# Optimization experiments

Hardware: AMD Instinct MI355X
Metric: run time of the kernel (lower is better)

## Reference

```python
import jax, jax.numpy as jnp
import numpy as np

K = 16  # neighbors
EPS = 1e-3  # Keras BatchNormalization default epsilon


def _bn(x, gamma, beta, mean, var):
    return (x - mean) * jax.lax.rsqrt(var + EPS) * gamma + beta


def setup_inputs() -> dict:
    key = jax.random.key(0)
    ks = jax.random.split(key, 16)
    B, P, C = 128, 256, 64
    inp = {
        "points": jax.random.normal(ks[0], (B, P, 3), jnp.float32),
        "features": jax.random.normal(ks[1], (B, P, C), jnp.float32),
        "w0": jax.random.normal(ks[2], (2 * C, 64), jnp.float32) * 0.08,
        "w1": jax.random.normal(ks[3], (64, 64), jnp.float32) * 0.12,
        "w2": jax.random.normal(ks[4], (64, 64), jnp.float32) * 0.12,
        "gammas": 0.8 + 0.4 * jax.random.uniform(ks[5], (3, 64), jnp.float32),
        "betas": 0.1 * jax.random.normal(ks[6], (3, 64), jnp.float32),
        "means": 0.1 * jax.random.normal(ks[7], (3, 64), jnp.float32),
        "variances": 0.5 + jax.random.uniform(ks[8], (3, 64), jnp.float32),
        "sc_w": jax.random.normal(ks[9], (C, 64), jnp.float32) * 0.12,
        "sc_gamma": 0.8 + 0.4 * jax.random.uniform(ks[10], (64,), jnp.float32),
        "sc_beta": 0.1 * jax.random.normal(ks[11], (64,), jnp.float32),
        "sc_mean": 0.1 * jax.random.normal(ks[12], (64,), jnp.float32),
        "sc_var": 0.5 + jax.random.uniform(ks[13], (64,), jnp.float32),
    }
    return inp


def reference(points, features, w0, w1, w2, gammas, betas, means, variances,
              sc_w, sc_gamma, sc_beta, sc_mean, sc_var):
    B, P, C = features.shape
    # pairwise squared-distance matrix: ||a||^2 - 2 a.b + ||b||^2  -> [B, P, P]
    r = jnp.sum(points * points, axis=2, keepdims=True)  # [B, P, 1]
    m = jnp.einsum('bpc,bqc->bpq', points, points)
    d = r - 2.0 * m + jnp.swapaxes(r, 1, 2)
    # top_k of -d: K+1 nearest (incl. self at position 0), drop self
    _, idx = jax.lax.top_k(-d, K + 1)
    idx = idx[:, :, 1:]  # [B, P, K]
    # KNN gather of features
    knn_fts = features[jnp.arange(B)[:, None, None], idx]  # [B, P, K, C]
    center = jnp.broadcast_to(features[:, :, None, :], (B, P, K, C))
    x = jnp.concatenate([center, knn_fts - center], axis=-1)  # [B, P, K, 2C]
    # per-edge MLP: 1x1 conv + BN (inference) + relu
    for i, w in enumerate((w0, w1, w2)):
        x = jnp.einsum('bpkc,cd->bpkd', x, w)
        x = _bn(x, gammas[i], betas[i], means[i], variances[i])
        x = jax.nn.relu(x)
    fts = jnp.mean(x, axis=2)  # average pooling over neighbors -> [B, P, 64]
    # shortcut 1x1 conv + BN
    sc = jnp.einsum('bpc,cd->bpd', features, sc_w)
    sc = _bn(sc, sc_gamma, sc_beta, sc_mean, sc_var)
    return jax.nn.relu(sc + fts)
```

## Files before the change

kernel.cpp:

```cpp
#include <hip/hip_runtime.h>
#include <math.h>

#define NBATCH 128
#define NP 256
#define NC 64
#define KNN 16
#define EPSV 1e-3f

typedef __bf16 bf16_t;
typedef bf16_t bf16x8 __attribute__((ext_vector_type(8)));
typedef float f32x4 __attribute__((ext_vector_type(4)));
typedef unsigned short u16x4 __attribute__((ext_vector_type(4)));

static __device__ __forceinline__ f32x4 mfma16(bf16x8 a, bf16x8 b, f32x4 c) {
    return __builtin_amdgcn_mfma_f32_16x16x32_bf16(a, b, c, 0, 0, 0);
}
static __device__ __forceinline__ unsigned short f2bfu(float f) {
    union { bf16_t b; unsigned short u; } cv; cv.b = (bf16_t)f; return cv.u;
}
static __device__ __forceinline__ unsigned umin2(unsigned a, unsigned b) { return a < b ? a : b; }
static __device__ __forceinline__ unsigned umax2(unsigned a, unsigned b) { return a > b ? a : b; }

#define CFENCE() asm volatile("" ::: "memory")

#define INSERTK(k_)                                                   \
    do {                                                              \
        _Pragma("unroll")                                             \
        for (int ii = KNN - 1; ii >= 1; --ii)                         \
            bk[ii] = umin2(umax2((k_), bk[ii - 1]), bk[ii]);          \
        bk[0] = umin2((k_), bk[0]);                                   \
    } while (0)

__global__ __launch_bounds__(256) void knn_kernel(const float* __restrict__ points,
                                                  int* __restrict__ idx_out) {
    const int bb = blockIdx.x >> 1;
    const int qbase = (blockIdx.x & 1) * 128;
    const int t = threadIdx.x;
    const int qt = t & 127;
    const int half = t >> 7;
    const int p = qbase + qt;

    __shared__ __align__(16) float4 sp[NP];
    __shared__ unsigned sk[128][17];

    const float* pb = points + (size_t)bb * NP * 3;
    sp[t] = make_float4(pb[t * 3 + 0], pb[t * 3 + 1], pb[t * 3 + 2], 0.f);
    __syncthreads();

    const float4 qp = sp[p];
    unsigned bk[KNN];
#pragma unroll
    for (int i = 0; i < KNN; ++i) bk[i] = 0xFFFFFFFFu;

    const int cbase = half * 128;
#pragma unroll 4
    for (int c = 0; c < 128; ++c) {
        const int cand = cbase + c;
        const float4 P = sp[cand];
        const float dx = qp.x - P.x, dy = qp.y - P.y, dz = qp.z - P.z;
        const float d = fmaf(dx, dx, fmaf(dy, dy, dz * dz));
        unsigned key = (__float_as_uint(d) & 0xFFFFFF00u) | (unsigned)cand;
        key = (cand == p) ? 0xFFFFFFFFu : key;
        INSERTK(key);
    }

    if (half == 1) {
#pragma unroll
        for (int i = 0; i < KNN; ++i) sk[qt][i] = bk[i];
    }
    __syncthreads();
    if (half == 0) {
        for (int j = 0; j < KNN; ++j) {
            const unsigned key = sk[qt][j];
            if (key >= bk[KNN - 1]) break;
            INSERTK(key);
        }
        int* op = idx_out + ((size_t)bb * NP + p) * KNN;
#pragma unroll
        for (int i = 0; i < KNN; ++i) op[i] = (int)(bk[i] & 0xFFu);
    }
}

__global__ __launch_bounds__(256) void fcvt_kernel(const float* __restrict__ f,
                                                   unsigned short* __restrict__ o) {
    const int tid = blockIdx.x * 256 + threadIdx.x;
    const float4 a = ((const float4*)f)[tid * 2];
    const float4 b = ((const float4*)f)[tid * 2 + 1];
    union { unsigned short s[8]; uint4 v; } r;
    r.s[0] = f2bfu(a.x); r.s[1] = f2bfu(a.y); r.s[2] = f2bfu(a.z); r.s[3] = f2bfu(a.w);
    r.s[4] = f2bfu(b.x); r.s[5] = f2bfu(b.y); r.s[6] = f2bfu(b.z); r.s[7] = f2bfu(b.w);
    ((uint4*)o)[tid] = r.v;
}

__global__ __launch_bounds__(256) void prep_kernel(
    const float* __restrict__ w0, const float* __restrict__ w1,
    const float* __restrict__ w2, const float* __restrict__ sc_w,
    const float* __restrict__ gammas, const float* __restrict__ betas,
    const float* __restrict__ means, const float* __restrict__ variances,
    const float* __restrict__ sc_gamma, const float* __restrict__ sc_beta,
    const float* __restrict__ sc_mean, const float* __restrict__ sc_var,
    unsigned short* __restrict__ wsf, float* __restrict__ bnp)
{
    const int tid = blockIdx.x * 256 + threadIdx.x;
    if (tid < 20480) {
        const int region = tid >> 12;
        const int e2 = tid & 4095;
        const int f = e2 >> 9;
        const int r = e2 & 511;
        const int lane = r >> 3, j = r & 7;
        const int ks = f >> 2, t = f & 3;
        const int row = ks * 32 + (lane >> 4) * 8 + j;
        const int col = 4 * (lane & 15) + t;
        float v;
        if (region == 0)      v = w0[row * 64 + col] - w0[(64 + row) * 64 + col];
        else if (region == 1) v = w0[(64 + row) * 64 + col];
        else if (region == 2) v = w1[row * 64 + col];
        else if (region == 3) v = w2[row * 64 + col];
        else                  v = sc_w[row * 64 + col];
        wsf[tid] = f2bfu(v);
    } else {
        const int e = tid - 20480;
        if (e < 192) {
            float s = gammas[e] * rsqrtf(variances[e] + EPSV);
            bnp[e] = s;
            bnp[192 + e] = betas[e] - means[e] * s;
        } else if (e < 256) {
            const int d = e - 192;
            float s = sc_gamma[d] * rsqrtf(sc_var[d] + EPSV);
            bnp[384 + d] = s;
            bnp[448 + d] = sc_beta[d] - sc_mean[d] * s;
        }
    }
}

__global__ __launch_bounds__(256) void edge_kernel(
    const unsigned short* __restrict__ fbf, const int* __restrict__ knn_idx,
    const unsigned short* __restrict__ wsf, const float* __restrict__ bnp,
    float* __restrict__ out)
{
    __shared__ __align__(16) unsigned short slab[4][16 * 72];
    __shared__ __align__(16) float s0buf[4][8][64];
    __shared__ __align__(16) float ftsbuf[4][8][64];

    const int tid = threadIdx.x;
    const int wid = tid >> 6;
    const int l = tid & 63;
    const int i = l & 15;
    const int h = l >> 4;
    const int wg = (blockIdx.x & 7) * 128 + (blockIdx.x >> 3);
    const int p0 = (wg * 4 + wid) * 8;
    const int b = p0 >> 8;

    unsigned short* sl = slab[wid];

    const bf16x8* __restrict__ WV = (const bf16x8*)(wsf);
    const bf16x8* __restrict__ W0H = (const bf16x8*)(wsf + 4096);
    const bf16x8* __restrict__ W1 = (const bf16x8*)(wsf + 8192);
    const bf16x8* __restrict__ W2 = (const bf16x8*)(wsf + 12288);

    bf16x8 w0h[2][4], w1r[2][4], w2r[2][4];
#pragma unroll
    for (int ks = 0; ks < 2; ++ks)
#pragma unroll
        for (int t = 0; t < 4; ++t) {
            w0h[ks][t] = W0H[(ks * 4 + t) * 64 + l];
            w1r[ks][t] = W1[(ks * 4 + t) * 64 + l];
            w2r[ks][t] = W2[(ks * 4 + t) * 64 + l];
        }

    float4 scl[3], shf[3];
#pragma unroll
    for (int L = 0; L < 3; ++L) {
        scl[L] = *(const float4*)&bnp[L * 64 + 4 * i];
        shf[L] = *(const float4*)&bnp[192 + L * 64 + 4 * i];
    }

    {
        const unsigned short* cp = fbf + (size_t)(p0 + (i & 7)) * NC;
        bf16x8 a0 = *(const bf16x8*)(cp + 8 * h);
        bf16x8 a1 = *(const bf16x8*)(cp + 32 + 8 * h);
        f32x4 acc[4];
#pragma unroll
        for (int t = 0; t < 4; ++t) {
            f32x4 z = {0.f, 0.f, 0.f, 0.f};
            z = mfma16(a0, WV[t * 64 + l], z);
            acc[t] = mfma16(a1, WV[(4 + t) * 64 + l], z);
        }
        if (h < 2) {
#pragma unroll
            for (int r = 0; r < 4; ++r) {
                float4 v = make_float4(acc[0][r], acc[1][r], acc[2][r], acc[3][r]);
                *(float4*)&s0buf[wid][h * 4 + r][4 * i] = v;
            }
        }
    }
    int nks[8];
#pragma unroll
    for (int q = 0; q < 8; ++q) nks[q] = knn_idx[(size_t)(p0 + q) * KNN + i];
    CFENCE();

    bf16x8 fc0, fc1;
    {
        const unsigned short* sp = fbf + (size_t)(b * NP + nks[0]) * NC;
        fc0 = *(const bf16x8*)(sp + 8 * h);
        fc1 = *(const bf16x8*)(sp + 32 + 8 * h);
    }

#pragma unroll
    for (int q = 0; q < 8; ++q) {
        float4 s0q = *(const float4*)&s0buf[wid][q][4 * i];
        {
            f32x4 acc[4];
#pragma unroll
            for (int t = 0; t < 4; ++t) {
                f32x4 z = {0.f, 0.f, 0.f, 0.f};
                z = mfma16(fc0, w0h[0][t], z);
                acc[t] = mfma16(fc1, w0h[1][t], z);
            }
            const float* sp_ = (const float*)&s0q;
            const float* sc_ = (const float*)&scl[0];
            const float* sh_ = (const float*)&shf[0];
#pragma unroll
            for (int r = 0; r < 4; ++r) {
                u16x4 pk;
#pragma unroll
                for (int t = 0; t < 4; ++t)
                    pk[t] = f2bfu(fmaxf(fmaf(acc[t][r] + sp_[t], sc_[t], sh_[t]), 0.f));
                *(u16x4*)&sl[(h * 4 + r) * 72 + 4 * i] = pk;
            }
        }
        bf16x8 fn0, fn1;
        if (q < 7) {
            const unsigned short* sp = fbf + (size_t)(b * NP + nks[(q + 1) & 7]) * NC;
            fn0 = *(const bf16x8*)(sp + 8 * h);
            fn1 = *(const bf16x8*)(sp + 32 + 8 * h);
        }
        CFENCE();

        {
            bf16x8 x0 = *(const bf16x8*)(sl + i * 72 + h * 8);
            bf16x8 x1 = *(const bf16x8*)(sl + i * 72 + h * 8 + 32);
            f32x4 acc[4];
#pragma unroll
            for (int t = 0; t < 4; ++t) {
                f32x4 z = {0.f, 0.f, 0.f, 0.f};
                z = mfma16(x0, w1r[0][t], z);
                acc[t] = mfma16(x1, w1r[1][t], z);
            }
            const float* sc_ = (const float*)&scl[1];
            const float* sh_ = (const float*)&shf[1];
#pragma unroll
            for (int r = 0; r < 4; ++r) {
                u16x4 pk;
#pragma unroll
                for (int t = 0; t < 4; ++t)
                    pk[t] = f2bfu(fmaxf(fmaf(acc[t][r], sc_[t], sh_[t]), 0.f));
                *(u16x4*)&sl[(h * 4 + r) * 72 + 4 * i] = pk;
            }
        }
        CFENCE();

        {
            bf16x8 x0 = *(const bf16x8*)(sl + i * 72 + h * 8);
            bf16x8 x1 = *(const bf16x8*)(sl + i * 72 + h * 8 + 32);
            const float* sc_ = (const float*)&scl[2];
            const float* sh_ = (const float*)&shf[2];
            float st[4];
#pragma unroll
            for (int t = 0; t < 4; ++t) {
                f32x4 z = {0.f, 0.f, 0.f, 0.f};
                z = mfma16(x0, w2r[0][t], z);
                f32x4 acc = mfma16(x1, w2r[1][t], z);
                float s = 0.f;
#pragma unroll
                for (int r = 0; r < 4; ++r)
                    s += fmaxf(fmaf(acc[r], sc_[t], sh_[t]), 0.f);
                s += __shfl_xor(s, 16, 64);
                s += __shfl_xor(s, 32, 64);
                st[t] = s * (1.f / 16.f);
            }
            if (h == 0)
                *(float4*)&ftsbuf[wid][q][4 * i] =
                    make_float4(st[0], st[1], st[2], st[3]);
        }
        CFENCE();
        fc0 = fn0; fc1 = fn1;
    }

    {
        const bf16x8* __restrict__ WS = (const bf16x8*)(wsf + 16384);
        float4 sscl = *(const float4*)&bnp[384 + 4 * i];
        float4 sshf = *(const float4*)&bnp[448 + 4 * i];
        const unsigned short* fp = fbf + (size_t)(p0 + (i & 7)) * NC;
        bf16x8 a0 = *(const bf16x8*)(fp + 8 * h);
        bf16x8 a1 = *(const bf16x8*)(fp + 32 + 8 * h);
        f32x4 acc[4];
#pragma unroll
        for (int t = 0; t < 4; ++t) {
            f32x4 z = {0.f, 0.f, 0.f, 0.f};
            z = mfma16(a0, WS[t * 64 + l], z);
            acc[t] = mfma16(a1, WS[(4 + t) * 64 + l], z);
        }
        if (h < 2) {
            const float* ss_ = (const float*)&sscl;
            const float* sf_ = (const float*)&sshf;
#pragma unroll
            for (int r = 0; r < 4; ++r) {
                const int q = h * 4 + r;
                float4 fts = *(const float4*)&ftsbuf[wid][q][4 * i];
                const float* ft_ = (const float*)&fts;
                float4 o;
                float* o_ = (float*)&o;
#pragma unroll
                for (int t = 0; t < 4; ++t)
                    o_[t] = fmaxf(fmaf(acc[t][r], ss_[t], sf_[t]) + ft_[t], 0.f);
                *(float4*)&out[(size_t)(p0 + q) * NC + 4 * i] = o;
            }
        }
    }
}

extern "C" void kernel_launch(void* const* d_in, const int* in_sizes, int n_in,
                              void* d_out, int out_size, void* d_ws, size_t ws_size,
                              hipStream_t stream) {
    const float* points    = (const float*)d_in[0];
    const float* features  = (const float*)d_in[1];
    const float* w0        = (const float*)d_in[2];
    const float* w1        = (const float*)d_in[3];
    const float* w2        = (const float*)d_in[4];
    const float* gammas    = (const float*)d_in[5];
    const float* betas     = (const float*)d_in[6];
    const float* means     = (const float*)d_in[7];
    const float* variances = (const float*)d_in[8];
    const float* sc_w      = (const float*)d_in[9];
    const float* sc_gamma  = (const float*)d_in[10];
    const float* sc_beta   = (const float*)d_in[11];
    const float* sc_mean   = (const float*)d_in[12];
    const float* sc_var    = (const float*)d_in[13];
    float* out = (float*)d_out;

    int* knn_buf = (int*)d_ws;
    unsigned short* fbf = (unsigned short*)((char*)d_ws + (1 << 21));
    unsigned short* wsf = (unsigned short*)((char*)d_ws + (3 << 21));
    float* bnp = (float*)((char*)d_ws + (3 << 21) + 40960);

    prep_kernel<<<81, 256, 0, stream>>>(w0, w1, w2, sc_w, gammas, betas, means,
                                        variances, sc_gamma, sc_beta, sc_mean,
                                        sc_var, wsf, bnp);
    fcvt_kernel<<<1024, 256, 0, stream>>>(features, fbf);
    knn_kernel<<<NBATCH * 2, 256, 0, stream>>>(points, knn_buf);
    edge_kernel<<<NBATCH * NP / 32, 256, 0, stream>>>(fbf, knn_buf, wsf, bnp, out);
}
```

Baseline: 52.70 us.

## Merge setup kernels into one launch and process point pairs in edge kernel

Three preparatory kernels (weight/BN prep, feature bf16 conversion, KNN search) are combined into one launch whose work is split by block index, cutting launch overhead and letting the independent pieces run concurrently. The edge kernel now handles two points per iteration, loading both neighbor sets up front and interleaving their MFMA chains through a double LDS slab, which exposes more instruction-level parallelism. The single-point software prefetch of the next point's neighbors is dropped, and the pair processing raises register and LDS use, which could lower occupancy.

```diff
diff --git a/kernel.cpp b/kernel.cpp
--- a/kernel.cpp
+++ b/kernel.cpp
@@ -31,104 +31,103 @@
         bk[0] = umin2((k_), bk[0]);                                   \
     } while (0)
 
-__global__ __launch_bounds__(256) void knn_kernel(const float* __restrict__ points,
-                                                  int* __restrict__ idx_out) {
-    const int bb = blockIdx.x >> 1;
-    const int qbase = (blockIdx.x & 1) * 128;
-    const int t = threadIdx.x;
-    const int qt = t & 127;
-    const int half = t >> 7;
-    const int p = qbase + qt;
-
-    __shared__ __align__(16) float4 sp[NP];
-    __shared__ unsigned sk[128][17];
-
-    const float* pb = points + (size_t)bb * NP * 3;
-    sp[t] = make_float4(pb[t * 3 + 0], pb[t * 3 + 1], pb[t * 3 + 2], 0.f);
-    __syncthreads();
-
-    const float4 qp = sp[p];
-    unsigned bk[KNN];
-#pragma unroll
-    for (int i = 0; i < KNN; ++i) bk[i] = 0xFFFFFFFFu;
-
-    const int cbase = half * 128;
-#pragma unroll 4
-    for (int c = 0; c < 128; ++c) {
-        const int cand = cbase + c;
-        const float4 P = sp[cand];
-        const float dx = qp.x - P.x, dy = qp.y - P.y, dz = qp.z - P.z;
-        const float d = fmaf(dx, dx, fmaf(dy, dy, dz * dz));
-        unsigned key = (__float_as_uint(d) & 0xFFFFFF00u) | (unsigned)cand;
-        key = (cand == p) ? 0xFFFFFFFFu : key;
-        INSERTK(key);
-    }
-
-    if (half == 1) {
-#pragma unroll
-        for (int i = 0; i < KNN; ++i) sk[qt][i] = bk[i];
-    }
-    __syncthreads();
-    if (half == 0) {
-        for (int j = 0; j < KNN; ++j) {
-            const unsigned key = sk[qt][j];
-            if (key >= bk[KNN - 1]) break;
-            INSERTK(key);
-        }
-        int* op = idx_out + ((size_t)bb * NP + p) * KNN;
-#pragma unroll
-        for (int i = 0; i < KNN; ++i) op[i] = (int)(bk[i] & 0xFFu);
-    }
-}
-
-__global__ __launch_bounds__(256) void fcvt_kernel(const float* __restrict__ f,
-                                                   unsigned short* __restrict__ o) {
-    const int tid = blockIdx.x * 256 + threadIdx.x;
-    const float4 a = ((const float4*)f)[tid * 2];
-    const float4 b = ((const float4*)f)[tid * 2 + 1];
-    union { unsigned short s[8]; uint4 v; } r;
-    r.s[0] = f2bfu(a.x); r.s[1] = f2bfu(a.y); r.s[2] = f2bfu(a.z); r.s[3] = f2bfu(a.w);
-    r.s[4] = f2bfu(b.x); r.s[5] = f2bfu(b.y); r.s[6] = f2bfu(b.z); r.s[7] = f2bfu(b.w);
-    ((uint4*)o)[tid] = r.v;
-}
-
-__global__ __launch_bounds__(256) void prep_kernel(
+__global__ __launch_bounds__(256) void setup_kernel(
+    const float* __restrict__ points, const float* __restrict__ features,
     const float* __restrict__ w0, const float* __restrict__ w1,
     const float* __restrict__ w2, const float* __restrict__ sc_w,
     const float* __restrict__ gammas, const float* __restrict__ betas,
     const float* __restrict__ means, const float* __restrict__ variances,
     const float* __restrict__ sc_gamma, const float* __restrict__ sc_beta,
     const float* __restrict__ sc_mean, const float* __restrict__ sc_var,
-    unsigned short* __restrict__ wsf, float* __restrict__ bnp)
+    unsigned short* __restrict__ fbf, unsigned short* __restrict__ wsf,
+    float* __restrict__ bnp, int* __restrict__ knn_out)
 {
-    const int tid = blockIdx.x * 256 + threadIdx.x;
-    if (tid < 20480) {
-        const int region = tid >> 12;
-        const int e2 = tid & 4095;
-        const int f = e2 >> 9;
-        const int r = e2 & 511;
-        const int lane = r >> 3, j = r & 7;
-        const int ks = f >> 2, t = f & 3;
-        const int row = ks * 32 + (lane >> 4) * 8 + j;
-        const int col = 4 * (lane & 15) + t;
-        float v;
-        if (region == 0)      v = w0[row * 64 + col] - w0[(64 + row) * 64 + col];
-        else if (region == 1) v = w0[(64 + row) * 64 + col];
-        else if (region == 2) v = w1[row * 64 + col];
-        else if (region == 3) v = w2[row * 64 + col];
-        else                  v = sc_w[row * 64 + col];
-        wsf[tid] = f2bfu(v);
+    const int bid = blockIdx.x;
+    if (bid < 1024) {
+        const int tid = bid * 256 + threadIdx.x;
+        const float4 a = ((const float4*)features)[tid * 2];
+        const float4 b = ((const float4*)features)[tid * 2 + 1];
+        union { unsigned short s[8]; uint4 v; } r;
+        r.s[0] = f2bfu(a.x); r.s[1] = f2bfu(a.y); r.s[2] = f2bfu(a.z); r.s[3] = f2bfu(a.w);
+        r.s[4] = f2bfu(b.x); r.s[5] = f2bfu(b.y); r.s[6] = f2bfu(b.z); r.s[7] = f2bfu(b.w);
+        ((uint4*)fbf)[tid] = r.v;
+    } else if (bid < 1105) {
+        const int tid = (bid - 1024) * 256 + threadIdx.x;
+        if (tid < 20480) {
+            const int region = tid >> 12;
+            const int e2 = tid & 4095;
+            const int f = e2 >> 9;
+            const int r = e2 & 511;
+            const int lane = r >> 3, j = r & 7;
+            const int ks = f >> 2, t = f & 3;
+            const int row = ks * 32 + (lane >> 4) * 8 + j;
+            const int col = 4 * (lane & 15) + t;
+            float v;
+            if (region == 0)      v = w0[row * 64 + col] - w0[(64 + row) * 64 + col];
+            else if (region == 1) v = w0[(64 + row) * 64 + col];
+            else if (region == 2) v = w1[row * 64 + col];
+            else if (region == 3) v = w2[row * 64 + col];
+            else                  v = sc_w[row * 64 + col];
+            wsf[tid] = f2bfu(v);
+        } else {
+            const int e = tid - 20480;
+            if (e < 192) {
+                float s = gammas[e] * rsqrtf(variances[e] + EPSV);
+                bnp[e] = s;
+                bnp[192 + e] = betas[e] - means[e] * s;
+            } else if (e < 256) {
+                const int d = e - 192;
+                float s = sc_gamma[d] * rsqrtf(sc_var[d] + EPSV);
+                bnp[384 + d] = s;
+                bnp[448 + d] = sc_beta[d] - sc_mean[d] * s;
+            }
+        }
     } else {
-        const int e = tid - 20480;
-        if (e < 192) {
-            float s = gammas[e] * rsqrtf(variances[e] + EPSV);
-            bnp[e] = s;
-            bnp[192 + e] = betas[e] - means[e] * s;
-        } else if (e < 256) {
-            const int d = e - 192;
-            float s = sc_gamma[d] * rsqrtf(sc_var[d] + EPSV);
-            bnp[384 + d] = s;
-            bnp[448 + d] = sc_beta[d] - sc_mean[d] * s;
+        __shared__ __align__(16) float4 sp[NP];
+        __shared__ unsigned sk[128][17];
+        const int kb = bid - 1105;
+        const int bb = kb >> 1;
+        const int qbase = (kb & 1) * 128;
+        const int t = threadIdx.x;
+        const int qt = t & 127;
+        const int half = t >> 7;
+        const int p = qbase + qt;
+
+        const float* pb = points + (size_t)bb * NP * 3;
+        sp[t] = make_float4(pb[t * 3 + 0], pb[t * 3 + 1], pb[t * 3 + 2], 0.f);
+        __syncthreads();
+
+        const float4 qp = sp[p];
+        unsigned bk[KNN];
+#pragma unroll
+        for (int i = 0; i < KNN; ++i) bk[i] = 0xFFFFFFFFu;
+
+        const int cbase = half * 128;
+#pragma unroll 4
+        for (int c = 0; c < 128; ++c) {
+            const int cand = cbase + c;
+            const float4 P = sp[cand];
+            const float dx = qp.x - P.x, dy = qp.y - P.y, dz = qp.z - P.z;
+            const float d = fmaf(dx, dx, fmaf(dy, dy, dz * dz));
+            unsigned key = (__float_as_uint(d) & 0xFFFFFF00u) | (unsigned)cand;
+            key = (cand == p) ? 0xFFFFFFFFu : key;
+            INSERTK(key);
+        }
+
+        if (half == 1) {
+#pragma unroll
+            for (int i = 0; i < KNN; ++i) sk[qt][i] = bk[i];
+        }
+        __syncthreads();
+        if (half == 0) {
+            for (int j = 0; j < KNN; ++j) {
+                const unsigned key = sk[qt][j];
+                if (key >= bk[KNN - 1]) break;
+                INSERTK(key);
+            }
+            int* op = knn_out + ((size_t)bb * NP + p) * KNN;
+#pragma unroll
+            for (int i = 0; i < KNN; ++i) op[i] = (int)(bk[i] & 0xFFu);
         }
     }
 }
@@ -138,7 +137,7 @@
     const unsigned short* __restrict__ wsf, const float* __restrict__ bnp,
     float* __restrict__ out)
 {
-    __shared__ __align__(16) unsigned short slab[4][16 * 72];
+    __shared__ __align__(16) unsigned short slab[4][2][16 * 72];
     __shared__ __align__(16) float s0buf[4][8][64];
     __shared__ __align__(16) float ftsbuf[4][8][64];
 
@@ -151,7 +150,8 @@
     const int p0 = (wg * 4 + wid) * 8;
     const int b = p0 >> 8;
 
-    unsigned short* sl = slab[wid];
+    unsigned short* sl0 = slab[wid][0];
+    unsigned short* sl1 = slab[wid][1];
 
     const bf16x8* __restrict__ WV = (const bf16x8*)(wsf);
     const bf16x8* __restrict__ W0H = (const bf16x8*)(wsf + 4096);
@@ -199,92 +199,133 @@
     for (int q = 0; q < 8; ++q) nks[q] = knn_idx[(size_t)(p0 + q) * KNN + i];
     CFENCE();
 
-    bf16x8 fc0, fc1;
-    {
-        const unsigned short* sp = fbf + (size_t)(b * NP + nks[0]) * NC;
-        fc0 = *(const bf16x8*)(sp + 8 * h);
-        fc1 = *(const bf16x8*)(sp + 32 + 8 * h);
-    }
-
-#pragma unroll
-    for (int q = 0; q < 8; ++q) {
-        float4 s0q = *(const float4*)&s0buf[wid][q][4 * i];
+#pragma unroll
+    for (int qp = 0; qp < 4; ++qp) {
+        const int q0 = 2 * qp, q1 = 2 * qp + 1;
+        bf16x8 f00, f01, f10, f11;
         {
-            f32x4 acc[4];
-#pragma unroll
-            for (int t = 0; t < 4; ++t) {
-                f32x4 z = {0.f, 0.f, 0.f, 0.f};
-                z = mfma16(fc0, w0h[0][t], z);
-                acc[t] = mfma16(fc1, w0h[1][t], z);
-            }
-            const float* sp_ = (const float*)&s0q;
+            const unsigned short* sp0 = fbf + (size_t)(b * NP + nks[q0]) * NC;
+            const unsigned short* sp1 = fbf + (size_t)(b * NP + nks[q1]) * NC;
+            f00 = *(const bf16x8*)(sp0 + 8 * h);
+            f01 = *(const bf16x8*)(sp0 + 32 + 8 * h);
+            f10 = *(const bf16x8*)(sp1 + 8 * h);
+            f11 = *(const bf16x8*)(sp1 + 32 + 8 * h);
+        }
+        {
+            float4 s0a = *(const float4*)&s0buf[wid][q0][4 * i];
             const float* sc_ = (const float*)&scl[0];
             const float* sh_ = (const float*)&shf[0];
+            f32x4 acc[4];
+#pragma unroll
+            for (int t = 0; t < 4; ++t) {
+                f32x4 z = {0.f, 0.f, 0.f, 0.f};
+                z = mfma16(f00, w0h[0][t], z);
+                acc[t] = mfma16(f01, w0h[1][t], z);
+            }
+            const float* sp_ = (const float*)&s0a;
 #pragma unroll
             for (int r = 0; r < 4; ++r) {
                 u16x4 pk;
 #pragma unroll
                 for (int t = 0; t < 4; ++t)
                     pk[t] = f2bfu(fmaxf(fmaf(acc[t][r] + sp_[t], sc_[t], sh_[t]), 0.f));
-                *(u16x4*)&sl[(h * 4 + r) * 72 + 4 * i] = pk;
-            }
-        }
-        bf16x8 fn0, fn1;
-        if (q < 7) {
-            const unsigned short* sp = fbf + (size_t)(b * NP + nks[(q + 1) & 7]) * NC;
-            fn0 = *(const bf16x8*)(sp + 8 * h);
-            fn1 = *(const bf16x8*)(sp + 32 + 8 * h);
+                *(u16x4*)&sl0[(h * 4 + r) * 72 + 4 * i] = pk;
+            }
+            float4 s0b = *(const float4*)&s0buf[wid][q1][4 * i];
+            const float* sq_ = (const float*)&s0b;
+#pragma unroll
+            for (int t = 0; t < 4; ++t) {
+                f32x4 z = {0.f, 0.f, 0.f, 0.f};
+                z = mfma16(f10, w0h[0][t], z);
+                acc[t] = mfma16(f11, w0h[1][t], z);
+            }
+#pragma unroll
+            for (int r = 0; r < 4; ++r) {
+                u16x4 pk;
+#pragma unroll
+                for (int t = 0; t < 4; ++t)
+                    pk[t] = f2bfu(fmaxf(fmaf(acc[t][r] + sq_[t], sc_[t], sh_[t]), 0.f));
+                *(u16x4*)&sl1[(h * 4 + r) * 72 + 4 * i] = pk;
+            }
         }
         CFENCE();
 
         {
-            bf16x8 x0 = *(const bf16x8*)(sl + i * 72 + h * 8);
-            bf16x8 x1 = *(const bf16x8*)(sl + i * 72 + h * 8 + 32);
-            f32x4 acc[4];
-#pragma unroll
-            for (int t = 0; t < 4; ++t) {
-                f32x4 z = {0.f, 0.f, 0.f, 0.f};
-                z = mfma16(x0, w1r[0][t], z);
-                acc[t] = mfma16(x1, w1r[1][t], z);
-            }
+            bf16x8 xa0 = *(const bf16x8*)(sl0 + i * 72 + h * 8);
+            bf16x8 xa1 = *(const bf16x8*)(sl0 + i * 72 + h * 8 + 32);
+            bf16x8 xb0 = *(const bf16x8*)(sl1 + i * 72 + h * 8);
+            bf16x8 xb1 = *(const bf16x8*)(sl1 + i * 72 + h * 8 + 32);
             const float* sc_ = (const float*)&scl[1];
             const float* sh_ = (const float*)&shf[1];
+            f32x4 acc[4];
+#pragma unroll
+            for (int t = 0; t < 4; ++t) {
+                f32x4 z = {0.f, 0.f, 0.f, 0.f};
+                z = mfma16(xa0, w1r[0][t], z);
+                acc[t] = mfma16(xa1, w1r[1][t], z);
+            }
 #pragma unroll
             for (int r = 0; r < 4; ++r) {
                 u16x4 pk;
 #pragma unroll
                 for (int t = 0; t < 4; ++t)
                     pk[t] = f2bfu(fmaxf(fmaf(acc[t][r], sc_[t], sh_[t]), 0.f));
-                *(u16x4*)&sl[(h * 4 + r) * 72 + 4 * i] = pk;
+                *(u16x4*)&sl0[(h * 4 + r) * 72 + 4 * i] = pk;
+            }
+#pragma unroll
+            for (int t = 0; t < 4; ++t) {
+                f32x4 z = {0.f, 0.f, 0.f, 0.f};
+                z = mfma16(xb0, w1r[0][t], z);
+                acc[t] = mfma16(xb1, w1r[1][t], z);
+            }
+#pragma unroll
+            for (int r = 0; r < 4; ++r) {
+                u16x4 pk;
+#pragma unroll
+                for (int t = 0; t < 4; ++t)
+                    pk[t] = f2bfu(fmaxf(fmaf(acc[t][r], sc_[t], sh_[t]), 0.f));
+                *(u16x4*)&sl1[(h * 4 + r) * 72 + 4 * i] = pk;
             }
         }
         CFENCE();
 
         {
-            bf16x8 x0 = *(const bf16x8*)(sl + i * 72 + h * 8);
-            bf16x8 x1 = *(const bf16x8*)(sl + i * 72 + h * 8 + 32);
+            bf16x8 xa0 = *(const bf16x8*)(sl0 + i * 72 + h * 8);
+            bf16x8 xa1 = *(const bf16x8*)(sl0 + i * 72 + h * 8 + 32);
+            bf16x8 xb0 = *(const bf16x8*)(sl1 + i * 72 + h * 8);
+            bf16x8 xb1 = *(const bf16x8*)(sl1 + i * 72 + h * 8 + 32);
             const float* sc_ = (const float*)&scl[2];
             const float* sh_ = (const float*)&shf[2];
-            float st[4];
-#pragma unroll
-            for (int t = 0; t < 4; ++t) {
-                f32x4 z = {0.f, 0.f, 0.f, 0.f};
-                z = mfma16(x0, w2r[0][t], z);
-                f32x4 acc = mfma16(x1, w2r[1][t], z);
+            float sa[4], sb[4];
+#pragma unroll
+            for (int t = 0; t < 4; ++t) {
+                f32x4 z = {0.f, 0.f, 0.f, 0.f};
+                z = mfma16(xa0, w2r[0][t], z);
+                f32x4 acc = mfma16(xa1, w2r[1][t], z);
                 float s = 0.f;
 #pragma unroll
                 for (int r = 0; r < 4; ++r)
                     s += fmaxf(fmaf(acc[r], sc_[t], sh_[t]), 0.f);
+                z = (f32x4){0.f, 0.f, 0.f, 0.f};
+                z = mfma16(xb0, w2r[0][t], z);
+                f32x4 accb = mfma16(xb1, w2r[1][t], z);
+                float sB = 0.f;
+#pragma unroll
+                for (int r = 0; r < 4; ++r)
+                    sB += fmaxf(fmaf(accb[r], sc_[t], sh_[t]), 0.f);
                 s += __shfl_xor(s, 16, 64);
                 s += __shfl_xor(s, 32, 64);
-                st[t] = s * (1.f / 16.f);
-            }
-            if (h == 0)
-                *(float4*)&ftsbuf[wid][q][4 * i] =
-                    make_float4(st[0], st[1], st[2], st[3]);
+                sB += __shfl_xor(sB, 16, 64);
+                sB += __shfl_xor(sB, 32, 64);
+                sa[t] = s * (1.f / 16.f);
+                sb[t] = sB * (1.f / 16.f);
+            }
+            if (h == 0) {
+                *(float4*)&ftsbuf[wid][q0][4 * i] = make_float4(sa[0], sa[1], sa[2], sa[3]);
+                *(float4*)&ftsbuf[wid][q1][4 * i] = make_float4(sb[0], sb[1], sb[2], sb[3]);
+            }
         }
         CFENCE();
-        fc0 = fn0; fc1 = fn1;
     }
 
     {
@@ -344,10 +385,9 @@
     unsigned short* wsf = (unsigned short*)((char*)d_ws + (3 << 21));
     float* bnp = (float*)((char*)d_ws + (3 << 21) + 40960);
 
-    prep_kernel<<<81, 256, 0, stream>>>(w0, w1, w2, sc_w, gammas, betas, means,
-                                        variances, sc_gamma, sc_beta, sc_mean,
-                                        sc_var, wsf, bnp);
-    fcvt_kernel<<<1024, 256, 0, stream>>>(features, fbf);
-    knn_kernel<<<NBATCH * 2, 256, 0, stream>>>(points, knn_buf);
+    setup_kernel<<<1361, 256, 0, stream>>>(points, features, w0, w1, w2, sc_w,
+                                           gammas, betas, means, variances,
+                                           sc_gamma, sc_beta, sc_mean, sc_var,
+                                           fbf, wsf, bnp, knn_buf);
     edge_kernel<<<NBATCH * NP / 32, 256, 0, stream>>>(fbf, knn_buf, wsf, bnp, out);
 }
```

Result: faster. 48.40 us (-8.2%).

## Merge prep, convert and KNN kernels into one launch; stage MLP weights in LDS

Applied to the files above, without the earlier changes.

The three independent setup kernels (weight/BN prep, feature bf16 conversion, KNN search) are combined into a single launch that dispatches on block index, removing two launch gaps and letting the stages overlap on the GPU. In the edge kernel, the per-lane register copies of the layer weights are replaced by a block-wide copy into shared memory, read at each MFMA. This lowers register pressure and may raise occupancy, but adds a __syncthreads, 24 KB of LDS per block, and LDS reads inside the inner loops. Combining the setup work also gives one kernel the KNN blocks' shared-memory footprint.

```diff
diff --git a/kernel.cpp b/kernel.cpp
--- a/kernel.cpp
+++ b/kernel.cpp
@@ -31,104 +31,103 @@
         bk[0] = umin2((k_), bk[0]);                                   \
     } while (0)
 
-__global__ __launch_bounds__(256) void knn_kernel(const float* __restrict__ points,
-                                                  int* __restrict__ idx_out) {
-    const int bb = blockIdx.x >> 1;
-    const int qbase = (blockIdx.x & 1) * 128;
-    const int t = threadIdx.x;
-    const int qt = t & 127;
-    const int half = t >> 7;
-    const int p = qbase + qt;
-
-    __shared__ __align__(16) float4 sp[NP];
-    __shared__ unsigned sk[128][17];
-
-    const float* pb = points + (size_t)bb * NP * 3;
-    sp[t] = make_float4(pb[t * 3 + 0], pb[t * 3 + 1], pb[t * 3 + 2], 0.f);
-    __syncthreads();
-
-    const float4 qp = sp[p];
-    unsigned bk[KNN];
-#pragma unroll
-    for (int i = 0; i < KNN; ++i) bk[i] = 0xFFFFFFFFu;
-
-    const int cbase = half * 128;
-#pragma unroll 4
-    for (int c = 0; c < 128; ++c) {
-        const int cand = cbase + c;
-        const float4 P = sp[cand];
-        const float dx = qp.x - P.x, dy = qp.y - P.y, dz = qp.z - P.z;
-        const float d = fmaf(dx, dx, fmaf(dy, dy, dz * dz));
-        unsigned key = (__float_as_uint(d) & 0xFFFFFF00u) | (unsigned)cand;
-        key = (cand == p) ? 0xFFFFFFFFu : key;
-        INSERTK(key);
-    }
-
-    if (half == 1) {
-#pragma unroll
-        for (int i = 0; i < KNN; ++i) sk[qt][i] = bk[i];
-    }
-    __syncthreads();
-    if (half == 0) {
-        for (int j = 0; j < KNN; ++j) {
-            const unsigned key = sk[qt][j];
-            if (key >= bk[KNN - 1]) break;
-            INSERTK(key);
-        }
-        int* op = idx_out + ((size_t)bb * NP + p) * KNN;
-#pragma unroll
-        for (int i = 0; i < KNN; ++i) op[i] = (int)(bk[i] & 0xFFu);
-    }
-}
-
-__global__ __launch_bounds__(256) void fcvt_kernel(const float* __restrict__ f,
-                                                   unsigned short* __restrict__ o) {
-    const int tid = blockIdx.x * 256 + threadIdx.x;
-    const float4 a = ((const float4*)f)[tid * 2];
-    const float4 b = ((const float4*)f)[tid * 2 + 1];
-    union { unsigned short s[8]; uint4 v; } r;
-    r.s[0] = f2bfu(a.x); r.s[1] = f2bfu(a.y); r.s[2] = f2bfu(a.z); r.s[3] = f2bfu(a.w);
-    r.s[4] = f2bfu(b.x); r.s[5] = f2bfu(b.y); r.s[6] = f2bfu(b.z); r.s[7] = f2bfu(b.w);
-    ((uint4*)o)[tid] = r.v;
-}
-
-__global__ __launch_bounds__(256) void prep_kernel(
+__global__ __launch_bounds__(256) void setup_kernel(
+    const float* __restrict__ points, const float* __restrict__ features,
     const float* __restrict__ w0, const float* __restrict__ w1,
     const float* __restrict__ w2, const float* __restrict__ sc_w,
     const float* __restrict__ gammas, const float* __restrict__ betas,
     const float* __restrict__ means, const float* __restrict__ variances,
     const float* __restrict__ sc_gamma, const float* __restrict__ sc_beta,
     const float* __restrict__ sc_mean, const float* __restrict__ sc_var,
-    unsigned short* __restrict__ wsf, float* __restrict__ bnp)
+    unsigned short* __restrict__ fbf, unsigned short* __restrict__ wsf,
+    float* __restrict__ bnp, int* __restrict__ knn_out)
 {
-    const int tid = blockIdx.x * 256 + threadIdx.x;
-    if (tid < 20480) {
-        const int region = tid >> 12;
-        const int e2 = tid & 4095;
-        const int f = e2 >> 9;
-        const int r = e2 & 511;
-        const int lane = r >> 3, j = r & 7;
-        const int ks = f >> 2, t = f & 3;
-        const int row = ks * 32 + (lane >> 4) * 8 + j;
-        const int col = 4 * (lane & 15) + t;
-        float v;
-        if (region == 0)      v = w0[row * 64 + col] - w0[(64 + row) * 64 + col];
-        else if (region == 1) v = w0[(64 + row) * 64 + col];
-        else if (region == 2) v = w1[row * 64 + col];
-        else if (region == 3) v = w2[row * 64 + col];
-        else                  v = sc_w[row * 64 + col];
-        wsf[tid] = f2bfu(v);
+    const int bid = blockIdx.x;
+    if (bid < 1024) {
+        const int tid = bid * 256 + threadIdx.x;
+        const float4 a = ((const float4*)features)[tid * 2];
+        const float4 b = ((const float4*)features)[tid * 2 + 1];
+        union { unsigned short s[8]; uint4 v; } r;
+        r.s[0] = f2bfu(a.x); r.s[1] = f2bfu(a.y); r.s[2] = f2bfu(a.z); r.s[3] = f2bfu(a.w);
+        r.s[4] = f2bfu(b.x); r.s[5] = f2bfu(b.y); r.s[6] = f2bfu(b.z); r.s[7] = f2bfu(b.w);
+        ((uint4*)fbf)[tid] = r.v;
+    } else if (bid < 1105) {
+        const int tid = (bid - 1024) * 256 + threadIdx.x;
+        if (tid < 20480) {
+            const int region = tid >> 12;
+            const int e2 = tid & 4095;
+            const int f = e2 >> 9;
+            const int r = e2 & 511;
+            const int lane = r >> 3, j = r & 7;
+            const int ks = f >> 2, t = f & 3;
+            const int row = ks * 32 + (lane >> 4) * 8 + j;
+            const int col = 4 * (lane & 15) + t;
+            float v;
+            if (region == 0)      v = w0[row * 64 + col] - w0[(64 + row) * 64 + col];
+            else if (region == 1) v = w0[(64 + row) * 64 + col];
+            else if (region == 2) v = w1[row * 64 + col];
+            else if (region == 3) v = w2[row * 64 + col];
+            else                  v = sc_w[row * 64 + col];
+            wsf[tid] = f2bfu(v);
+        } else {
+            const int e = tid - 20480;
+            if (e < 192) {
+                float s = gammas[e] * rsqrtf(variances[e] + EPSV);
+                bnp[e] = s;
+                bnp[192 + e] = betas[e] - means[e] * s;
+            } else if (e < 256) {
+                const int d = e - 192;
+                float s = sc_gamma[d] * rsqrtf(sc_var[d] + EPSV);
+                bnp[384 + d] = s;
+                bnp[448 + d] = sc_beta[d] - sc_mean[d] * s;
+            }
+        }
     } else {
-        const int e = tid - 20480;
-        if (e < 192) {
-            float s = gammas[e] * rsqrtf(variances[e] + EPSV);
-            bnp[e] = s;
-            bnp[192 + e] = betas[e] - means[e] * s;
-        } else if (e < 256) {
-            const int d = e - 192;
-            float s = sc_gamma[d] * rsqrtf(sc_var[d] + EPSV);
-            bnp[384 + d] = s;
-            bnp[448 + d] = sc_beta[d] - sc_mean[d] * s;
+        __shared__ __align__(16) float4 sp[NP];
+        __shared__ unsigned sk[128][17];
+        const int kb = bid - 1105;
+        const int bb = kb >> 1;
+        const int qbase = (kb & 1) * 128;
+        const int t = threadIdx.x;
+        const int qt = t & 127;
+        const int half = t >> 7;
+        const int p = qbase + qt;
+
+        const float* pb = points + (size_t)bb * NP * 3;
+        sp[t] = make_float4(pb[t * 3 + 0], pb[t * 3 + 1], pb[t * 3 + 2], 0.f);
+        __syncthreads();
+
+        const float4 qp = sp[p];
+        unsigned bk[KNN];
+#pragma unroll
+        for (int i = 0; i < KNN; ++i) bk[i] = 0xFFFFFFFFu;
+
+        const int cbase = half * 128;
+#pragma unroll 4
+        for (int c = 0; c < 128; ++c) {
+            const int cand = cbase + c;
+            const float4 P = sp[cand];
+            const float dx = qp.x - P.x, dy = qp.y - P.y, dz = qp.z - P.z;
+            const float d = fmaf(dx, dx, fmaf(dy, dy, dz * dz));
+            unsigned key = (__float_as_uint(d) & 0xFFFFFF00u) | (unsigned)cand;
+            key = (cand == p) ? 0xFFFFFFFFu : key;
+            INSERTK(key);
+        }
+
+        if (half == 1) {
+#pragma unroll
+            for (int i = 0; i < KNN; ++i) sk[qt][i] = bk[i];
+        }
+        __syncthreads();
+        if (half == 0) {
+            for (int j = 0; j < KNN; ++j) {
+                const unsigned key = sk[qt][j];
+                if (key >= bk[KNN - 1]) break;
+                INSERTK(key);
+            }
+            int* op = knn_out + ((size_t)bb * NP + p) * KNN;
+#pragma unroll
+            for (int i = 0; i < KNN; ++i) op[i] = (int)(bk[i] & 0xFFu);
         }
     }
 }
@@ -138,6 +137,7 @@
     const unsigned short* __restrict__ wsf, const float* __restrict__ bnp,
     float* __restrict__ out)
 {
+    __shared__ __align__(16) unsigned short wlds[24 * 512];
     __shared__ __align__(16) unsigned short slab[4][16 * 72];
     __shared__ __align__(16) float s0buf[4][8][64];
     __shared__ __align__(16) float ftsbuf[4][8][64];
@@ -153,20 +153,14 @@
 
     unsigned short* sl = slab[wid];
 
-    const bf16x8* __restrict__ WV = (const bf16x8*)(wsf);
-    const bf16x8* __restrict__ W0H = (const bf16x8*)(wsf + 4096);
-    const bf16x8* __restrict__ W1 = (const bf16x8*)(wsf + 8192);
-    const bf16x8* __restrict__ W2 = (const bf16x8*)(wsf + 12288);
-
-    bf16x8 w0h[2][4], w1r[2][4], w2r[2][4];
-#pragma unroll
-    for (int ks = 0; ks < 2; ++ks)
-#pragma unroll
-        for (int t = 0; t < 4; ++t) {
-            w0h[ks][t] = W0H[(ks * 4 + t) * 64 + l];
-            w1r[ks][t] = W1[(ks * 4 + t) * 64 + l];
-            w2r[ks][t] = W2[(ks * 4 + t) * 64 + l];
-        }
+    {
+        const uint4* src = (const uint4*)(wsf + 4096);
+        uint4* dst = (uint4*)wlds;
+#pragma unroll
+        for (int k = 0; k < 6; ++k) dst[tid + k * 256] = src[tid + k * 256];
+    }
+
+    #define WF(fi_) (*(const bf16x8*)&wlds[(fi_) * 512 + l * 8])
 
     float4 scl[3], shf[3];
 #pragma unroll
@@ -176,6 +170,7 @@
     }
 
     {
+        const bf16x8* __restrict__ WV = (const bf16x8*)(wsf);
         const unsigned short* cp = fbf + (size_t)(p0 + (i & 7)) * NC;
         bf16x8 a0 = *(const bf16x8*)(cp + 8 * h);
         bf16x8 a1 = *(const bf16x8*)(cp + 32 + 8 * h);
@@ -197,7 +192,8 @@
     int nks[8];
 #pragma unroll
     for (int q = 0; q < 8; ++q) nks[q] = knn_idx[(size_t)(p0 + q) * KNN + i];
-    CFENCE();
+
+    __syncthreads();
 
     bf16x8 fc0, fc1;
     {
@@ -214,8 +210,8 @@
 #pragma unroll
             for (int t = 0; t < 4; ++t) {
                 f32x4 z = {0.f, 0.f, 0.f, 0.f};
-                z = mfma16(fc0, w0h[0][t], z);
-                acc[t] = mfma16(fc1, w0h[1][t], z);
+                z = mfma16(fc0, WF(t), z);
+                acc[t] = mfma16(fc1, WF(4 + t), z);
             }
             const float* sp_ = (const float*)&s0q;
             const float* sc_ = (const float*)&scl[0];
@@ -244,8 +240,8 @@
 #pragma unroll
             for (int t = 0; t < 4; ++t) {
                 f32x4 z = {0.f, 0.f, 0.f, 0.f};
-                z = mfma16(x0, w1r[0][t], z);
-                acc[t] = mfma16(x1, w1r[1][t], z);
+                z = mfma16(x0, WF(8 + t), z);
+                acc[t] = mfma16(x1, WF(12 + t), z);
             }
             const float* sc_ = (const float*)&scl[1];
             const float* sh_ = (const float*)&shf[1];
@@ -269,8 +265,8 @@
 #pragma unroll
             for (int t = 0; t < 4; ++t) {
                 f32x4 z = {0.f, 0.f, 0.f, 0.f};
-                z = mfma16(x0, w2r[0][t], z);
-                f32x4 acc = mfma16(x1, w2r[1][t], z);
+                z = mfma16(x0, WF(16 + t), z);
+                f32x4 acc = mfma16(x1, WF(20 + t), z);
                 float s = 0.f;
 #pragma unroll
                 for (int r = 0; r < 4; ++r)
@@ -318,6 +314,7 @@
             }
         }
     }
+    #undef WF
 }
 
 extern "C" void kernel_launch(void* const* d_in, const int* in_sizes, int n_in,
@@ -344,10 +341,9 @@
     unsigned short* wsf = (unsigned short*)((char*)d_ws + (3 << 21));
     float* bnp = (float*)((char*)d_ws + (3 << 21) + 40960);
 
-    prep_kernel<<<81, 256, 0, stream>>>(w0, w1, w2, sc_w, gammas, betas, means,
-                                        variances, sc_gamma, sc_beta, sc_mean,
-                                        sc_var, wsf, bnp);
-    fcvt_kernel<<<1024, 256, 0, stream>>>(features, fbf);
-    knn_kernel<<<NBATCH * 2, 256, 0, stream>>>(points, knn_buf);
+    setup_kernel<<<1361, 256, 0, stream>>>(points, features, w0, w1, w2, sc_w,
+                                           gammas, betas, means, variances,
+                                           sc_gamma, sc_beta, sc_mean, sc_var,
+                                           fbf, wsf, bnp, knn_buf);
     edge_kernel<<<NBATCH * NP / 32, 256, 0, stream>>>(fbf, knn_buf, wsf, bnp, out);
 }
```

Measured after the change: 46.99 us. 1.12x faster.
